# Kernel tuning notes

Measured on AMD Instinct MI355X. Metric: run time of the kernel, lower is better.

The kernel has to match this reference:

```python
import jax, jax.numpy as jnp
import numpy as np

N_NODES = 10000

def setup_inputs() -> dict:
    key = jax.random.key(0)
    k1, k2, k3, k4 = jax.random.split(key, 4)
    N, E, D, H = N_NODES, 320000, 128, 256
    x = jax.random.normal(k1, (N, D), dtype=jnp.float32)
    edge_index = jax.random.randint(k2, (2, E), 0, N, dtype=jnp.int32)
    edge_weight = jax.random.uniform(k3, (E,), dtype=jnp.float32)
    W_enc = jax.random.normal(k4, (D, H), dtype=jnp.float32) * 0.05
    return {"x": x, "edge_index": edge_index, "edge_weight": edge_weight, "W_enc": W_enc}

def _random_walk_matrix(edge_index, edge_weight, num_nodes):
    # sparse COO -> dense (coalescing duplicate edges by summation, as torch does)
    adj = jnp.zeros((num_nodes, num_nodes), dtype=edge_weight.dtype)
    adj = adj.at[edge_index[0], edge_index[1]].add(edge_weight)
    # faithful to original: adj / (adj.sum(dim=1) + eps), broadcasting over last axis
    return adj / (adj.sum(axis=1) + 1e-20)

def reference(x, edge_index, edge_weight, W_enc):
    num_nodes = x.shape[0]
    # augmentors are identity: (x1, ei1, ew1) == (x2, ei2, ew2) == inputs
    rw1 = _random_walk_matrix(edge_index, edge_weight, num_nodes)
    rw2 = rw1
    # encoder modeled as a single linear map (opaque GNN submodule stub)
    z = x @ W_enc
    z1 = z
    z2 = z
    return (z, z1, z2, rw1, rw2)
```

## Files before the change

### kernel.cpp

```cpp
#include <hip/hip_runtime.h>
#include <hip/hip_bf16.h>

#define N_NODES 10000
#define N_EDGES 320000
#define DIM_D   128
#define DIM_H   256

#define Z_ELEMS   (N_NODES * DIM_H)
#define RW_ELEMS  ((size_t)N_NODES * N_NODES)
#define OFF_Z1    ((size_t)Z_ELEMS)
#define OFF_Z2    ((size_t)2 * Z_ELEMS)
#define OFF_RW1   ((size_t)3 * Z_ELEMS)
#define OFF_RW2   (OFF_RW1 + RW_ELEMS)

#define WS_ROWSUM 0
#define WS_CNT    40960
#define WS_COLP   81920
#define WS_VALP   5201920
#define ELL_K     128

#define GEMM_RB 79
#define GEMM_CB 4
#define GEMM_TOTAL (GEMM_RB * GEMM_CB)
#define RW_BLOCKS (2 * N_NODES)

typedef float f32x4 __attribute__((ext_vector_type(4)));

__device__ inline void nt_store4(float* p, float x, float y, float z, float w) {
    f32x4 t = {x, y, z, w};
    __builtin_nontemporal_store(t, (f32x4*)p);
}

__global__ void init_kernel(float4* __restrict__ ws) {
    int i = blockIdx.x * blockDim.x + threadIdx.x;
    ws[i] = make_float4(0.f, 0.f, 0.f, 0.f);
}

__global__ void build_kernel(const int* __restrict__ ei,
                             const float* __restrict__ ew,
                             float* __restrict__ rowsum,
                             int* __restrict__ cnt,
                             int* __restrict__ colp,
                             float* __restrict__ valp, int E) {
    int e = blockIdx.x * blockDim.x + threadIdx.x;
    if (e >= E) return;
    int s = ei[e];
    int d = ei[E + e];
    float w = ew[e];
    atomicAdd(&rowsum[s], w);
    int slot = atomicAdd(&cnt[s], 1);
    if (slot < ELL_K) {
        colp[s * ELL_K + slot] = d;
        valp[s * ELL_K + slot] = w;
    }
}

__global__ __launch_bounds__(512) void fused_kernel(
        const float* __restrict__ rowsum,
        const int* __restrict__ cnt,
        const int* __restrict__ colp,
        const float* __restrict__ valp,
        float* __restrict__ rw1,
        float* __restrict__ rw2,
        const float* __restrict__ x,
        const float* __restrict__ W,
        float* __restrict__ out) {
    __shared__ float smem[N_NODES];
    int t = threadIdx.x;

    if (blockIdx.x < RW_BLOCKS) {
        int b = blockIdx.x;
        int r = b >> 1;
        float* dst = ((b & 1) ? rw2 : rw1) + (size_t)r * N_NODES;

        float4* row4 = reinterpret_cast<float4*>(smem);
        const float4 z4 = make_float4(0.f, 0.f, 0.f, 0.f);
        row4[t]        = z4;
        row4[t + 512]  = z4;
        row4[t + 1024] = z4;
        row4[t + 1536] = z4;
        if (t < 452) row4[t + 2048] = z4;
        __syncthreads();

        int n = cnt[r];
        if (n > ELL_K) n = ELL_K;
        if (t < n) {
            int d  = colp[r * ELL_K + t];
            float w = valp[r * ELL_K + t];
            atomicAdd(&smem[d], w / (rowsum[d] + 1e-20f));
        }
        __syncthreads();

        float4 v;
        v = row4[t];        nt_store4(dst + 4 * t,          v.x, v.y, v.z, v.w);
        v = row4[t + 512];  nt_store4(dst + 4 * (t + 512),  v.x, v.y, v.z, v.w);
        v = row4[t + 1024]; nt_store4(dst + 4 * (t + 1024), v.x, v.y, v.z, v.w);
        v = row4[t + 1536]; nt_store4(dst + 4 * (t + 1536), v.x, v.y, v.z, v.w);
        if (t < 452) {
            v = row4[t + 2048]; nt_store4(dst + 4 * (t + 2048), v.x, v.y, v.z, v.w);
        }
        return;
    }

    float* xs  = smem;
    float* wsm = smem + 128 * 33;

    int bid = blockIdx.x - RW_BLOCKS;
    int rb = bid >> 2;
    int cb = bid & 3;
    int r_base = rb * 128;
    int c_base = cb * 64;

    int tr = t >> 4;
    int tc = t & 15;

    float acc[4][4];
#pragma unroll
    for (int i = 0; i < 4; ++i)
#pragma unroll
        for (int j = 0; j < 4; ++j) acc[i][j] = 0.f;

    for (int k0 = 0; k0 < DIM_D; k0 += 32) {
#pragma unroll
        for (int q = t; q < 1024; q += 512) {
            int row = q >> 3;
            int c4  = q & 7;
            int grow = r_base + row;
            float4 f = (grow < N_NODES)
                ? *reinterpret_cast<const float4*>(x + (size_t)grow * DIM_D + k0 + c4 * 4)
                : make_float4(0.f, 0.f, 0.f, 0.f);
            float* dstp = xs + row * 33 + c4 * 4;
            dstp[0] = f.x; dstp[1] = f.y; dstp[2] = f.z; dstp[3] = f.w;
        }
        {
            int kk = t >> 4;
            int c4 = t & 15;
            float4 f = *reinterpret_cast<const float4*>(
                W + (size_t)(k0 + kk) * DIM_H + c_base + c4 * 4);
            *reinterpret_cast<float4*>(wsm + kk * 64 + c4 * 4) = f;
        }
        __syncthreads();

        for (int kk = 0; kk < 32; ++kk) {
            float4 w4 = *reinterpret_cast<const float4*>(wsm + kk * 64 + tc * 4);
#pragma unroll
            for (int i = 0; i < 4; ++i) {
                float a = xs[(tr * 4 + i) * 33 + kk];
                acc[i][0] += a * w4.x;
                acc[i][1] += a * w4.y;
                acc[i][2] += a * w4.z;
                acc[i][3] += a * w4.w;
            }
        }
        __syncthreads();
    }

#pragma unroll
    for (int i = 0; i < 4; ++i) {
        int row = r_base + tr * 4 + i;
        if (row >= N_NODES) continue;
        size_t o = (size_t)row * DIM_H + c_base + tc * 4;
        nt_store4(out + o,          acc[i][0], acc[i][1], acc[i][2], acc[i][3]);
        nt_store4(out + OFF_Z1 + o, acc[i][0], acc[i][1], acc[i][2], acc[i][3]);
        nt_store4(out + OFF_Z2 + o, acc[i][0], acc[i][1], acc[i][2], acc[i][3]);
    }
}

extern "C" void kernel_launch(void* const* d_in, const int* in_sizes, int n_in,
                              void* d_out, int out_size, void* d_ws, size_t ws_size,
                              hipStream_t stream) {
    const float* x      = (const float*)d_in[0];
    const int*   ei     = (const int*)d_in[1];
    const float* ew     = (const float*)d_in[2];
    const float* W_enc  = (const float*)d_in[3];
    float* out = (float*)d_out;

    char* ws = (char*)d_ws;
    float* rowsum = (float*)(ws + WS_ROWSUM);
    int*   cnt    = (int*)(ws + WS_CNT);
    int*   colp   = (int*)(ws + WS_COLP);
    float* valp   = (float*)(ws + WS_VALP);

    init_kernel<<<10, 512, 0, stream>>>(reinterpret_cast<float4*>(ws));

    build_kernel<<<(N_EDGES + 511) / 512, 512, 0, stream>>>(
        ei, ew, rowsum, cnt, colp, valp, N_EDGES);

    fused_kernel<<<RW_BLOCKS + GEMM_TOTAL, 512, 0, stream>>>(
        rowsum, cnt, colp, valp, out + OFF_RW1, out + OFF_RW2, x, W_enc, out);
}
```

Baseline: 212.9 us.

## Split dense rw output into bulk zero-fill plus sparse patch kernel

Replaces the per-row shared-memory build of each dense random-walk row with a grid-stride bulk zero fill of both rw matrices, run alongside the GEMM blocks. A separate small kernel then writes only the nonzero entries, deduplicating repeated columns with an O(n^2) scan in shared memory. This removes the large shared-memory footprint and per-row scatter, and turns the 800MB output into a plain streaming store. The cost is an extra launch and plain stores in place of nontemporal ones.

```diff
diff --git a/kernel.cpp b/kernel.cpp
--- a/kernel.cpp
+++ b/kernel.cpp
@@ -22,7 +22,10 @@
 #define GEMM_RB 79
 #define GEMM_CB 4
 #define GEMM_TOTAL (GEMM_RB * GEMM_CB)
-#define RW_BLOCKS (2 * N_NODES)
+
+#define FILL_BLOCKS 4096
+#define FILL_UNITS  12500000ull
+#define UNITS_PER_PASS ((size_t)FILL_BLOCKS * 512)
 
 typedef float f32x4 __attribute__((ext_vector_type(4)));
 
@@ -55,49 +58,25 @@
     }
 }
 
-__global__ __launch_bounds__(512) void fused_kernel(
-        const float* __restrict__ rowsum,
-        const int* __restrict__ cnt,
-        const int* __restrict__ colp,
-        const float* __restrict__ valp,
-        float* __restrict__ rw1,
-        float* __restrict__ rw2,
+__global__ __launch_bounds__(512) void fill_gemm_kernel(
+        float* __restrict__ rw,
         const float* __restrict__ x,
         const float* __restrict__ W,
         float* __restrict__ out) {
-    __shared__ float smem[N_NODES];
+    __shared__ float smem[128 * 33 + 32 * 64];
     int t = threadIdx.x;
 
-    if (blockIdx.x < RW_BLOCKS) {
-        int b = blockIdx.x;
-        int r = b >> 1;
-        float* dst = ((b & 1) ? rw2 : rw1) + (size_t)r * N_NODES;
-
-        float4* row4 = reinterpret_cast<float4*>(smem);
+    if (blockIdx.x >= GEMM_TOTAL) {
+        size_t b = blockIdx.x - GEMM_TOTAL;
+        float4* p = reinterpret_cast<float4*>(rw);
         const float4 z4 = make_float4(0.f, 0.f, 0.f, 0.f);
-        row4[t]        = z4;
-        row4[t + 512]  = z4;
-        row4[t + 1024] = z4;
-        row4[t + 1536] = z4;
-        if (t < 452) row4[t + 2048] = z4;
-        __syncthreads();
-
-        int n = cnt[r];
-        if (n > ELL_K) n = ELL_K;
-        if (t < n) {
-            int d  = colp[r * ELL_K + t];
-            float w = valp[r * ELL_K + t];
-            atomicAdd(&smem[d], w / (rowsum[d] + 1e-20f));
-        }
-        __syncthreads();
-
-        float4 v;
-        v = row4[t];        nt_store4(dst + 4 * t,          v.x, v.y, v.z, v.w);
-        v = row4[t + 512];  nt_store4(dst + 4 * (t + 512),  v.x, v.y, v.z, v.w);
-        v = row4[t + 1024]; nt_store4(dst + 4 * (t + 1024), v.x, v.y, v.z, v.w);
-        v = row4[t + 1536]; nt_store4(dst + 4 * (t + 1536), v.x, v.y, v.z, v.w);
-        if (t < 452) {
-            v = row4[t + 2048]; nt_store4(dst + 4 * (t + 2048), v.x, v.y, v.z, v.w);
+#pragma unroll
+        for (int pass = 0; pass < 6; ++pass) {
+            size_t u = (size_t)pass * UNITS_PER_PASS + b * 512 + t;
+            if (u < FILL_UNITS) {
+                float4* q = p + 4 * u;
+                q[0] = z4; q[1] = z4; q[2] = z4; q[3] = z4;
+            }
         }
         return;
     }
@@ -105,7 +84,7 @@
     float* xs  = smem;
     float* wsm = smem + 128 * 33;
 
-    int bid = blockIdx.x - RW_BLOCKS;
+    int bid = blockIdx.x;
     int rb = bid >> 2;
     int cb = bid & 3;
     int r_base = rb * 128;
@@ -166,6 +145,45 @@
     }
 }
 
+__global__ __launch_bounds__(64) void patch_kernel(
+        const float* __restrict__ rowsum,
+        const int* __restrict__ cnt,
+        const int* __restrict__ colp,
+        const float* __restrict__ valp,
+        float* __restrict__ rw1,
+        float* __restrict__ rw2) {
+    __shared__ int   cols[ELL_K];
+    __shared__ float vals[ELL_K];
+    int r = blockIdx.x;
+    int t = threadIdx.x;
+
+    int n = cnt[r];
+    if (n > ELL_K) n = ELL_K;
+    for (int i = t; i < n; i += 64) {
+        cols[i] = colp[r * ELL_K + i];
+        vals[i] = valp[r * ELL_K + i];
+    }
+    __syncthreads();
+
+    size_t base = (size_t)r * N_NODES;
+    for (int i = t; i < n; i += 64) {
+        int c = cols[i];
+        float sum = 0.f;
+        int first = i;
+        for (int j = 0; j < n; ++j) {
+            if (cols[j] == c) {
+                sum += vals[j];
+                if (j < first) first = j;
+            }
+        }
+        if (first == i) {
+            float v = sum / (rowsum[c] + 1e-20f);
+            rw1[base + c] = v;
+            rw2[base + c] = v;
+        }
+    }
+}
+
 extern "C" void kernel_launch(void* const* d_in, const int* in_sizes, int n_in,
                               void* d_out, int out_size, void* d_ws, size_t ws_size,
                               hipStream_t stream) {
@@ -186,6 +204,9 @@
     build_kernel<<<(N_EDGES + 511) / 512, 512, 0, stream>>>(
         ei, ew, rowsum, cnt, colp, valp, N_EDGES);
 
-    fused_kernel<<<RW_BLOCKS + GEMM_TOTAL, 512, 0, stream>>>(
-        rowsum, cnt, colp, valp, out + OFF_RW1, out + OFF_RW2, x, W_enc, out);
-}
+    fill_gemm_kernel<<<GEMM_TOTAL + FILL_BLOCKS, 512, 0, stream>>>(
+        out + OFF_RW1, x, W_enc, out);
+
+    patch_kernel<<<N_NODES, 64, 0, stream>>>(
+        rowsum, cnt, colp, valp, out + OFF_RW1, out + OFF_RW2);
+}
```

Result: slower. 316.6 us (+48.7%).

## Build RW rows from sparse flags without full-row shared buffer, one block per row

Applied to the files above, without the earlier changes.

Replaces the 40KB per-block shared dense row with a small buffer of edge columns and values plus a bitmask per float4 slot. Each thread emits its float4 chunks directly, scanning the edge list only when its chunk is flagged, and writes both rw1 and rw2 from one block. The GEMM blocks move to the front of the grid. The smaller shared footprint allows more resident blocks and halves the RW block count, at the cost of a serial scan over the row's edges for flagged chunks.

```diff
diff --git a/kernel.cpp b/kernel.cpp
--- a/kernel.cpp
+++ b/kernel.cpp
@@ -22,7 +22,6 @@
 #define GEMM_RB 79
 #define GEMM_CB 4
 #define GEMM_TOTAL (GEMM_RB * GEMM_CB)
-#define RW_BLOCKS (2 * N_NODES)
 
 typedef float f32x4 __attribute__((ext_vector_type(4)));
 
@@ -65,39 +64,56 @@
         const float* __restrict__ x,
         const float* __restrict__ W,
         float* __restrict__ out) {
-    __shared__ float smem[N_NODES];
+    __shared__ float smem[128 * 33 + 32 * 64];
     int t = threadIdx.x;
 
-    if (blockIdx.x < RW_BLOCKS) {
-        int b = blockIdx.x;
-        int r = b >> 1;
-        float* dst = ((b & 1) ? rw2 : rw1) + (size_t)r * N_NODES;
-
-        float4* row4 = reinterpret_cast<float4*>(smem);
-        const float4 z4 = make_float4(0.f, 0.f, 0.f, 0.f);
-        row4[t]        = z4;
-        row4[t + 512]  = z4;
-        row4[t + 1024] = z4;
-        row4[t + 1536] = z4;
-        if (t < 452) row4[t + 2048] = z4;
+    if (blockIdx.x >= GEMM_TOTAL) {
+        int r = blockIdx.x - GEMM_TOTAL;
+
+        int*   cols  = reinterpret_cast<int*>(smem);
+        float* vals  = smem + 128;
+        int*   flags = reinterpret_cast<int*>(smem + 256);
+
+        flags[t] = 0;
         __syncthreads();
 
         int n = cnt[r];
         if (n > ELL_K) n = ELL_K;
         if (t < n) {
-            int d  = colp[r * ELL_K + t];
+            int c   = colp[r * ELL_K + t];
             float w = valp[r * ELL_K + t];
-            atomicAdd(&smem[d], w / (rowsum[d] + 1e-20f));
-        }
-        __syncthreads();
-
-        float4 v;
-        v = row4[t];        nt_store4(dst + 4 * t,          v.x, v.y, v.z, v.w);
-        v = row4[t + 512];  nt_store4(dst + 4 * (t + 512),  v.x, v.y, v.z, v.w);
-        v = row4[t + 1024]; nt_store4(dst + 4 * (t + 1024), v.x, v.y, v.z, v.w);
-        v = row4[t + 1536]; nt_store4(dst + 4 * (t + 1536), v.x, v.y, v.z, v.w);
-        if (t < 452) {
-            v = row4[t + 2048]; nt_store4(dst + 4 * (t + 2048), v.x, v.y, v.z, v.w);
+            cols[t] = c;
+            vals[t] = w / (rowsum[c] + 1e-20f);
+            int f4 = c >> 2;
+            atomicOr(&flags[f4 & 511], 1 << (f4 >> 9));
+        }
+        __syncthreads();
+
+        int fl = flags[t];
+        float* d1 = rw1 + (size_t)r * N_NODES;
+        float* d2 = rw2 + (size_t)r * N_NODES;
+
+#pragma unroll
+        for (int p = 0; p < 5; ++p) {
+            int f4 = t + 512 * p;
+            if (p == 4 && t >= 452) break;
+            float a0 = 0.f, a1 = 0.f, a2 = 0.f, a3 = 0.f;
+            if (fl & (1 << p)) {
+                for (int j = 0; j < n; ++j) {
+                    int c = cols[j];
+                    if ((c >> 2) == f4) {
+                        float v = vals[j];
+                        switch (c & 3) {
+                            case 0: a0 += v; break;
+                            case 1: a1 += v; break;
+                            case 2: a2 += v; break;
+                            default: a3 += v; break;
+                        }
+                    }
+                }
+            }
+            nt_store4(d1 + 4 * f4, a0, a1, a2, a3);
+            nt_store4(d2 + 4 * f4, a0, a1, a2, a3);
         }
         return;
     }
@@ -105,7 +121,7 @@
     float* xs  = smem;
     float* wsm = smem + 128 * 33;
 
-    int bid = blockIdx.x - RW_BLOCKS;
+    int bid = blockIdx.x;
     int rb = bid >> 2;
     int cb = bid & 3;
     int r_base = rb * 128;
@@ -186,6 +202,6 @@
     build_kernel<<<(N_EDGES + 511) / 512, 512, 0, stream>>>(
         ei, ew, rowsum, cnt, colp, valp, N_EDGES);
 
-    fused_kernel<<<RW_BLOCKS + GEMM_TOTAL, 512, 0, stream>>>(
+    fused_kernel<<<GEMM_TOTAL + N_NODES, 512, 0, stream>>>(
         rowsum, cnt, colp, valp, out + OFF_RW1, out + OFF_RW2, x, W_enc, out);
 }
```

Measured after the change: 272.6 us. 1.28x slower.
